# Optimization experiments

Hardware: AMD Instinct MI355X
Metric: run time of the kernel (lower is better)

The kernel has to match this reference:

```python
import jax, jax.numpy as jnp
import numpy as np

BN_EPS = 1e-5


def _knn_idx(pos, k):
    # pos: (B, 3, N). Nearest-k by squared euclidean distance (self included).
    sq = jnp.sum(pos * pos, axis=1)                        # (B, N)
    inner = jnp.einsum('bcn,bcm->bnm', pos, pos)           # (B, N, N)
    neg_dist = 2.0 * inner - sq[:, :, None] - sq[:, None, :]
    _, idx = jax.lax.top_k(neg_dist, k)                    # (B, N, k)
    return idx


def setup_inputs() -> dict:
    key = jax.random.key(0)
    k1, k2, k3 = jax.random.split(key, 3)
    B, C, N, K, D = 4, 64, 8192, 16, 64
    return {
        'x': jax.random.normal(k1, (B, C, N), dtype=jnp.float32),
        'pos': jax.random.normal(k2, (B, 3, N), dtype=jnp.float32),
        'spectral_filter': jax.random.normal(k3, (K, C, D), dtype=jnp.float32),
        'gamma': jnp.ones((D,), dtype=jnp.float32),
        'beta': jnp.zeros((D,), dtype=jnp.float32),
    }


def reference(x, pos, spectral_filter, gamma, beta):
    k = spectral_filter.shape[0]
    idx = _knn_idx(pos, k)                                  # (B, N, k) int32
    # gather neighbors: nb[b, c, n, j] = x[b, c, idx[b, n, j]]
    nb = jax.vmap(lambda xf, ii: xf[:, ii])(x, idx)         # (B, C, N, k)
    edge = nb - x[:, :, :, None]                            # (B, C, N, k)
    # per-k small GEMM: 'bnkc,kcd->bnd' (channel dim is axis 1 here)
    out = jnp.einsum('bcnk,kcd->bnd', edge, spectral_filter)
    out = out.transpose(0, 2, 1)                            # (B, D, N)
    # BatchNorm1d, training mode (biased variance over batch and points)
    mean = jnp.mean(out, axis=(0, 2), keepdims=True)
    var = jnp.var(out, axis=(0, 2), keepdims=True)
    out = (out - mean) * jax.lax.rsqrt(var + BN_EPS)
    return out * gamma[None, :, None] + beta[None, :, None]
```

## Files before the change

kernel.cpp:

```cpp
#include <hip/hip_runtime.h>
#include <hip/hip_bf16.h>

#define NPTS 8192
#define NQ   32768
#define KNN  16
#define SCAP 112

#define OFF_XT   0
#define OFF_FBIG (8*1024*1024)
#define OFF_SUMS (OFF_FBIG + 278528)
#define OFF_IDX  (OFF_SUMS + 512)
#define OFF_PRE  (OFF_IDX + 2*1024*1024)
#define OFF_SQ   OFF_PRE

__device__ __forceinline__ float sq3(float x, float y, float z) {
    #pragma clang fp contract(off)
    float xx = x * x;
    float yy = y * y;
    float zz = z * z;
    return (xx + yy) + zz;
}
__device__ __forceinline__ float negd2(float qx, float qy, float qz, float sqn,
                                       float mx, float my, float mz, float sqm) {
    #pragma clang fp contract(off)
    float p0 = qx * mx;
    float inn = __builtin_fmaf(qz, mz, __builtin_fmaf(qy, my, p0));
    float t = 2.0f * inn;
    float u = t - sqn;
    return u - sqm;
}
#define KEY_EPS2 2.0e-3f

__global__ __launch_bounds__(256) void k_prep(const float* __restrict__ x,
                                              const float* __restrict__ F,
                                              const float* __restrict__ pos,
                                              float* __restrict__ xT,
                                              float* __restrict__ Fb,
                                              float* __restrict__ sums,
                                              float* __restrict__ sqa) {
    int bid = blockIdx.x;
    if (bid < 512) {
        __shared__ float tile[64][65];
        int lane = threadIdx.x & 63, wid = threadIdx.x >> 6;
        int b = bid >> 7, nt = bid & 127;
        int n0 = nt * 64;
        for (int rr = 0; rr < 16; ++rr) {
            int c = wid * 16 + rr;
            tile[c][lane] = x[((size_t)b * 64 + c) * NPTS + n0 + lane];
        }
        __syncthreads();
        for (int rr = 0; rr < 16; ++rr) {
            int r = wid * 16 + rr;
            xT[((size_t)(b * NPTS + n0 + r)) * 64 + lane] = tile[lane][r];
        }
    } else if (bid < 528) {
        int j = bid - 512;
        for (int e = threadIdx.x; e < 4096; e += 256)
            Fb[j * 4096 + e] = F[j * 4096 + e];
    } else if (bid == 528) {
        for (int e = threadIdx.x; e < 4096; e += 256) {
            float s = 0.f;
            for (int k = 0; k < 16; ++k) s += F[k * 4096 + e];
            Fb[16 * 4096 + e] = -s;
        }
    } else if (bid == 529) {
        if (threadIdx.x < 128) sums[threadIdx.x] = 0.f;
    } else {
        int g = (bid - 530) * 256 + threadIdx.x;
        int b = g >> 13, n = g & (NPTS - 1);
        const float* pb = pos + (size_t)b * 3 * NPTS;
        sqa[g] = sq3(pb[n], pb[NPTS + n], pb[2 * NPTS + n]);
    }
}

__global__ __launch_bounds__(256, 8) void k_knn(const float* __restrict__ pos,
                                                const float* __restrict__ sqa,
                                                int* __restrict__ idxo) {
    __shared__ int            cnt[16];
    __shared__ unsigned short sidx[16][SCAP];
    __shared__ float          skey[16][SCAP];
    __shared__ int            outI[16][16];
    int t = threadIdx.x, lane = t & 63, wid = t >> 6;
    int qblk = blockIdx.x * 16;
    int b = qblk >> 13;
    const float* px = pos + (size_t)b * 3 * NPTS;
    const float* py = px + NPTS;
    const float* pz = py + NPTS;
    const float* sb = sqa + (size_t)b * NPTS;
    int n0 = (qblk & (NPTS - 1)) + wid * 4;

    float qxs[4], qys[4], qzs[4], sqs[4], tqx[4], tqy[4], tqz[4];
    #pragma unroll
    for (int i = 0; i < 4; ++i) {
        qxs[i] = px[n0 + i]; qys[i] = py[n0 + i]; qzs[i] = pz[n0 + i];
        sqs[i] = sb[n0 + i];
        tqx[i] = 2.0f * qxs[i]; tqy[i] = 2.0f * qys[i]; tqz[i] = 2.0f * qzs[i];
    }
    if (lane < 4) cnt[wid * 4 + lane] = 0;
    if (lane < 16) {
        #pragma unroll
        for (int i = 0; i < 4; ++i) outI[wid * 4 + i][lane] = n0 + i;
    }

    float lm[4];
    #pragma unroll
    for (int i = 0; i < 4; ++i) lm[i] = -3.4e38f;
    for (int it = 0; it < 32; ++it) {
        int m = it * 256 + lane * 4;
        float4 X = *(const float4*)(px + m);
        float4 Y = *(const float4*)(py + m);
        float4 Z = *(const float4*)(pz + m);
        float4 S = *(const float4*)(sb + m);
        #pragma unroll
        for (int i = 0; i < 4; ++i) {
            float a0 = __builtin_fmaf(tqx[i], X.x, __builtin_fmaf(tqy[i], Y.x, __builtin_fmaf(tqz[i], Z.x, -S.x)));
            float a1 = __builtin_fmaf(tqx[i], X.y, __builtin_fmaf(tqy[i], Y.y, __builtin_fmaf(tqz[i], Z.y, -S.y)));
            float a2 = __builtin_fmaf(tqx[i], X.z, __builtin_fmaf(tqy[i], Y.z, __builtin_fmaf(tqz[i], Z.z, -S.z)));
            float a3 = __builtin_fmaf(tqx[i], X.w, __builtin_fmaf(tqy[i], Y.w, __builtin_fmaf(tqz[i], Z.w, -S.w)));
            float m012 = fmaxf(fmaxf(a0, a1), a2);
            lm[i] = fmaxf(fmaxf(m012, a3), lm[i]);
        }
    }

    float thr[4];
    {
        unsigned up[4], pfx[4];
        #pragma unroll
        for (int i = 0; i < 4; ++i) {
            unsigned s = __float_as_uint(lm[i]);
            up[i]  = s ^ ((unsigned)((int)s >> 31) | 0x80000000u);
            pfx[i] = 0u;
        }
        for (int bit = 31; bit >= 0; --bit) {
            unsigned bmask = 1u << bit;
            #pragma unroll
            for (int i = 0; i < 4; ++i) {
                unsigned trial = pfx[i] | bmask;
                unsigned long long m = __ballot(up[i] >= trial);
                if (__popcll(m) >= 16) pfx[i] = trial;
            }
        }
        #pragma unroll
        for (int i = 0; i < 4; ++i) {
            unsigned p = pfx[i];
            unsigned sbits = (p & 0x80000000u) ? (p ^ 0x80000000u) : ~p;
            thr[i] = __uint_as_float(sbits) - KEY_EPS2;
        }
    }

    for (int it = 0; it < 32; ++it) {
        int m = it * 256 + lane * 4;
        float4 X = *(const float4*)(px + m);
        float4 Y = *(const float4*)(py + m);
        float4 Z = *(const float4*)(pz + m);
        float4 S = *(const float4*)(sb + m);
        #pragma unroll
        for (int i = 0; i < 4; ++i) {
            int lq = wid * 4 + i;
            float a0 = __builtin_fmaf(tqx[i], X.x, __builtin_fmaf(tqy[i], Y.x, __builtin_fmaf(tqz[i], Z.x, -S.x)));
            float a1 = __builtin_fmaf(tqx[i], X.y, __builtin_fmaf(tqy[i], Y.y, __builtin_fmaf(tqz[i], Z.y, -S.y)));
            float a2 = __builtin_fmaf(tqx[i], X.z, __builtin_fmaf(tqy[i], Y.z, __builtin_fmaf(tqz[i], Z.z, -S.z)));
            float a3 = __builtin_fmaf(tqx[i], X.w, __builtin_fmaf(tqy[i], Y.w, __builtin_fmaf(tqz[i], Z.w, -S.w)));
            if (a0 >= thr[i]) { int s_ = atomicAdd(&cnt[lq],1); if (s_<SCAP) sidx[lq][s_] = (unsigned short)m; }
            if (a1 >= thr[i]) { int s_ = atomicAdd(&cnt[lq],1); if (s_<SCAP) sidx[lq][s_] = (unsigned short)(m+1); }
            if (a2 >= thr[i]) { int s_ = atomicAdd(&cnt[lq],1); if (s_<SCAP) sidx[lq][s_] = (unsigned short)(m+2); }
            if (a3 >= thr[i]) { int s_ = atomicAdd(&cnt[lq],1); if (s_<SCAP) sidx[lq][s_] = (unsigned short)(m+3); }
        }
    }

    #pragma unroll 1
    for (int i = 0; i < 4; ++i) {
        int lq = wid * 4 + i;
        int S = cnt[lq]; if (S > SCAP) S = SCAP;
        for (int p = lane; p < S; p += 64) {
            int m = sidx[lq][p];
            skey[lq][p] = negd2(qxs[i], qys[i], qzs[i], sqs[i],
                                px[m], py[m], pz[m], sb[m]);
        }
    }

    #pragma unroll 1
    for (int i = 0; i < 4; ++i) {
        int lq = wid * 4 + i;
        int S = cnt[lq]; if (S > SCAP) S = SCAP;
        for (int p = lane; p < S; p += 64) {
            int m = sidx[lq][p];
            float km = skey[lq][p];
            int rank = 0;
            for (int j = 0; j < S; ++j) {
                float kj = skey[lq][j];
                int ij = sidx[lq][j];
                if (kj > km || (kj == km && ij < m)) rank++;
            }
            if (rank < KNN) outI[lq][rank] = m;
        }
    }
    __syncthreads();
    {
        int lq = t >> 4;
        idxo[(size_t)(qblk + lq) * KNN + (t & 15)] = outI[lq][t & 15];
    }
}

#define CPAD 68
__global__ __launch_bounds__(256) void k_conv(const float* __restrict__ xT,
                                              const float* __restrict__ Fb,
                                              const int* __restrict__ idx,
                                              float* __restrict__ outp,
                                              float* __restrict__ sums) {
    __shared__ float At[64][CPAD];
    __shared__ float Bt[64 * 64];
    int t = threadIdx.x;
    int q0 = blockIdx.x * 64;
    int bbase = q0 & ~(NPTS - 1);
    int qi0 = (t >> 4) * 4;
    int dj0 = (t & 15) * 4;
    int r = t & 63;
    int s = t >> 6;

    float acc[4][4];
    #pragma unroll
    for (int a = 0; a < 4; ++a)
        #pragma unroll
        for (int bb = 0; bb < 4; ++bb) acc[a][bb] = 0.f;

    for (int j = 0; j < 17; ++j) {
        {
            int qg = q0 + r;
            int nbr = (j < 16) ? (idx[(size_t)qg * KNN + j] & (NPTS - 1))
                               : (qg & (NPTS - 1));
            const float* src = xT + ((size_t)(bbase + nbr) * 64 + s * 16);
            float4 v0 = *(const float4*)(src);
            float4 v1 = *(const float4*)(src + 4);
            float4 v2 = *(const float4*)(src + 8);
            float4 v3 = *(const float4*)(src + 12);
            int c0 = s * 16;
            At[c0+ 0][r] = v0.x; At[c0+ 1][r] = v0.y; At[c0+ 2][r] = v0.z; At[c0+ 3][r] = v0.w;
            At[c0+ 4][r] = v1.x; At[c0+ 5][r] = v1.y; At[c0+ 6][r] = v1.z; At[c0+ 7][r] = v1.w;
            At[c0+ 8][r] = v2.x; At[c0+ 9][r] = v2.y; At[c0+10][r] = v2.z; At[c0+11][r] = v2.w;
            At[c0+12][r] = v3.x; At[c0+13][r] = v3.y; At[c0+14][r] = v3.z; At[c0+15][r] = v3.w;
        }
        {
            const float* fj = Fb + j * 4096;
            #pragma unroll
            for (int u = 0; u < 4; ++u) {
                int e = u * 1024 + t * 4;
                *(float4*)&Bt[e] = *(const float4*)(fj + e);
            }
        }
        __syncthreads();
        #pragma unroll 8
        for (int k = 0; k < 64; ++k) {
            float4 av = *(const float4*)&At[k][qi0];
            float4 bv = *(const float4*)&Bt[k * 64 + dj0];
            acc[0][0] = fmaf(av.x, bv.x, acc[0][0]);
            acc[0][1] = fmaf(av.x, bv.y, acc[0][1]);
            acc[0][2] = fmaf(av.x, bv.z, acc[0][2]);
            acc[0][3] = fmaf(av.x, bv.w, acc[0][3]);
            acc[1][0] = fmaf(av.y, bv.x, acc[1][0]);
            acc[1][1] = fmaf(av.y, bv.y, acc[1][1]);
            acc[1][2] = fmaf(av.y, bv.z, acc[1][2]);
            acc[1][3] = fmaf(av.y, bv.w, acc[1][3]);
            acc[2][0] = fmaf(av.z, bv.x, acc[2][0]);
            acc[2][1] = fmaf(av.z, bv.y, acc[2][1]);
            acc[2][2] = fmaf(av.z, bv.z, acc[2][2]);
            acc[2][3] = fmaf(av.z, bv.w, acc[2][3]);
            acc[3][0] = fmaf(av.w, bv.x, acc[3][0]);
            acc[3][1] = fmaf(av.w, bv.y, acc[3][1]);
            acc[3][2] = fmaf(av.w, bv.z, acc[3][2]);
            acc[3][3] = fmaf(av.w, bv.w, acc[3][3]);
        }
        __syncthreads();
    }
    #pragma unroll
    for (int qi = 0; qi < 4; ++qi) {
        float4 o = make_float4(acc[qi][0], acc[qi][1], acc[qi][2], acc[qi][3]);
        *(float4*)(outp + (size_t)(q0 + qi0 + qi) * 64 + dj0) = o;
    }
    {
        float* P  = Bt;
        float* P2 = Bt + 1024;
        int g = t >> 4;
        #pragma unroll
        for (int dd = 0; dd < 4; ++dd) {
            float sv = ((acc[0][dd] + acc[1][dd]) + acc[2][dd]) + acc[3][dd];
            float qv = fmaf(acc[3][dd], acc[3][dd],
                       fmaf(acc[2][dd], acc[2][dd],
                       fmaf(acc[1][dd], acc[1][dd], acc[0][dd] * acc[0][dd])));
            P [g * 64 + dj0 + dd] = sv;
            P2[g * 64 + dj0 + dd] = qv;
        }
        __syncthreads();
        if (t < 64) {
            float a = 0.f, b2 = 0.f;
            #pragma unroll
            for (int gg = 0; gg < 16; ++gg) {
                a  += P [gg * 64 + t];
                b2 += P2[gg * 64 + t];
            }
            atomicAdd(&sums[t], a);
            atomicAdd(&sums[64 + t], b2);
        }
    }
}

__global__ __launch_bounds__(256) void k_bn(const float* __restrict__ outp,
                                            const float* __restrict__ sums,
                                            const float* __restrict__ gamma,
                                            const float* __restrict__ beta,
                                            float* __restrict__ out) {
    __shared__ float tile[64][65];
    __shared__ float sa[64], sb[64];
    int lane = threadIdx.x & 63, wid = threadIdx.x >> 6;
    int b = blockIdx.x >> 7, nt = blockIdx.x & 127;
    int n0 = nt * 64;
    if (threadIdx.x < 64) {
        const float inv = 1.f / 32768.f;
        float mean = sums[threadIdx.x] * inv;
        float var = sums[64 + threadIdx.x] * inv - mean * mean;
        float rs = rsqrtf(var + 1e-5f);
        float a = rs * gamma[threadIdx.x];
        sa[threadIdx.x] = a;
        sb[threadIdx.x] = beta[threadIdx.x] - mean * a;
    }
    for (int rr = 0; rr < 16; ++rr) {
        int r = wid * 16 + rr;
        tile[r][lane] = outp[((size_t)(b * NPTS + n0 + r)) * 64 + lane];
    }
    __syncthreads();
    for (int rr = 0; rr < 16; ++rr) {
        int dr = wid * 16 + rr;
        out[((size_t)b * 64 + dr) * NPTS + n0 + lane] =
            fmaf(tile[lane][dr], sa[dr], sb[dr]);
    }
}

extern "C" void kernel_launch(void* const* d_in, const int* in_sizes, int n_in,
                              void* d_out, int out_size, void* d_ws, size_t ws_size,
                              hipStream_t stream) {
    (void)in_sizes; (void)n_in; (void)out_size; (void)ws_size;
    const float* x     = (const float*)d_in[0];
    const float* pos   = (const float*)d_in[1];
    const float* F     = (const float*)d_in[2];
    const float* gamma = (const float*)d_in[3];
    const float* beta  = (const float*)d_in[4];
    float* out = (float*)d_out;

    char* ws = (char*)d_ws;
    float* xT   = (float*)(ws + OFF_XT);
    float* Fb   = (float*)(ws + OFF_FBIG);
    float* sums = (float*)(ws + OFF_SUMS);
    int*   idx  = (int*)(ws + OFF_IDX);
    float* pre  = (float*)(ws + OFF_PRE);
    float* sqa  = (float*)(ws + OFF_SQ);

    k_prep<<<658, 256, 0, stream>>>(x, F, pos, xT, Fb, sums, sqa);
    k_knn<<<2048, 256, 0, stream>>>(pos, sqa, idx);
    k_conv<<<512, 256, 0, stream>>>(xT, Fb, idx, pre, sums);
    k_bn<<<512, 256, 0, stream>>>(pre, sums, gamma, beta, out);
}
```

Baseline: 259.2 us.

## Fuse kNN threshold and collection passes with progressive threshold refinement

The kNN kernel used to make two full passes over all 8192 points: one to find per-lane maxima for a top-16 threshold, and one to collect candidates above it. Now only the first 1024 points set an initial threshold. A single pass over the rest then both collects candidates and keeps updating the lane maxima, recomputing the threshold at two later checkpoints. This roughly halves the global loads and FMA work of the scan. In exchange, early loose thresholds admit more candidates, so the candidate buffer grows from 112 to 160 entries, raising LDS use and risking overflow that would drop true neighbours.

```diff
diff --git a/kernel.cpp b/kernel.cpp
--- a/kernel.cpp
+++ b/kernel.cpp
@@ -4,7 +4,7 @@
 #define NPTS 8192
 #define NQ   32768
 #define KNN  16
-#define SCAP 112
+#define SCAP 160
 
 #define OFF_XT   0
 #define OFF_FBIG (8*1024*1024)
@@ -73,6 +73,31 @@
     }
 }
 
+__device__ __forceinline__ void sel16(const float* lm, float* thr) {
+    unsigned up[4], pfx[4];
+    #pragma unroll
+    for (int i = 0; i < 4; ++i) {
+        unsigned s = __float_as_uint(lm[i]);
+        up[i]  = s ^ ((unsigned)((int)s >> 31) | 0x80000000u);
+        pfx[i] = 0u;
+    }
+    for (int bit = 31; bit >= 0; --bit) {
+        unsigned bmask = 1u << bit;
+        #pragma unroll
+        for (int i = 0; i < 4; ++i) {
+            unsigned trial = pfx[i] | bmask;
+            unsigned long long m = __ballot(up[i] >= trial);
+            if (__popcll(m) >= 16) pfx[i] = trial;
+        }
+    }
+    #pragma unroll
+    for (int i = 0; i < 4; ++i) {
+        unsigned p = pfx[i];
+        unsigned sbits = (p & 0x80000000u) ? (p ^ 0x80000000u) : ~p;
+        thr[i] = __uint_as_float(sbits) - KEY_EPS2;
+    }
+}
+
 __global__ __launch_bounds__(256, 8) void k_knn(const float* __restrict__ pos,
                                                 const float* __restrict__ sqa,
                                                 int* __restrict__ idxo) {
@@ -89,12 +114,11 @@
     const float* sb = sqa + (size_t)b * NPTS;
     int n0 = (qblk & (NPTS - 1)) + wid * 4;
 
-    float qxs[4], qys[4], qzs[4], sqs[4], tqx[4], tqy[4], tqz[4];
-    #pragma unroll
-    for (int i = 0; i < 4; ++i) {
-        qxs[i] = px[n0 + i]; qys[i] = py[n0 + i]; qzs[i] = pz[n0 + i];
+    float sqs[4], tqx[4], tqy[4], tqz[4];
+    #pragma unroll
+    for (int i = 0; i < 4; ++i) {
         sqs[i] = sb[n0 + i];
-        tqx[i] = 2.0f * qxs[i]; tqy[i] = 2.0f * qys[i]; tqz[i] = 2.0f * qzs[i];
+        tqx[i] = 2.0f * px[n0 + i]; tqy[i] = 2.0f * py[n0 + i]; tqz[i] = 2.0f * pz[n0 + i];
     }
     if (lane < 4) cnt[wid * 4 + lane] = 0;
     if (lane < 16) {
@@ -105,7 +129,8 @@
     float lm[4];
     #pragma unroll
     for (int i = 0; i < 4; ++i) lm[i] = -3.4e38f;
-    for (int it = 0; it < 32; ++it) {
+
+    for (int it = 0; it < 4; ++it) {
         int m = it * 256 + lane * 4;
         float4 X = *(const float4*)(px + m);
         float4 Y = *(const float4*)(py + m);
@@ -123,32 +148,9 @@
     }
 
     float thr[4];
-    {
-        unsigned up[4], pfx[4];
-        #pragma unroll
-        for (int i = 0; i < 4; ++i) {
-            unsigned s = __float_as_uint(lm[i]);
-            up[i]  = s ^ ((unsigned)((int)s >> 31) | 0x80000000u);
-            pfx[i] = 0u;
-        }
-        for (int bit = 31; bit >= 0; --bit) {
-            unsigned bmask = 1u << bit;
-            #pragma unroll
-            for (int i = 0; i < 4; ++i) {
-                unsigned trial = pfx[i] | bmask;
-                unsigned long long m = __ballot(up[i] >= trial);
-                if (__popcll(m) >= 16) pfx[i] = trial;
-            }
-        }
-        #pragma unroll
-        for (int i = 0; i < 4; ++i) {
-            unsigned p = pfx[i];
-            unsigned sbits = (p & 0x80000000u) ? (p ^ 0x80000000u) : ~p;
-            thr[i] = __uint_as_float(sbits) - KEY_EPS2;
-        }
-    }
-
-    for (int it = 0; it < 32; ++it) {
+    sel16(lm, thr);
+
+    for (int it = 0; it < 4; ++it) {
         int m = it * 256 + lane * 4;
         float4 X = *(const float4*)(px + m);
         float4 Y = *(const float4*)(py + m);
@@ -168,13 +170,37 @@
         }
     }
 
+    for (int it = 4; it < 32; ++it) {
+        if (it == 8 || it == 16) sel16(lm, thr);
+        int m = it * 256 + lane * 4;
+        float4 X = *(const float4*)(px + m);
+        float4 Y = *(const float4*)(py + m);
+        float4 Z = *(const float4*)(pz + m);
+        float4 S = *(const float4*)(sb + m);
+        #pragma unroll
+        for (int i = 0; i < 4; ++i) {
+            int lq = wid * 4 + i;
+            float a0 = __builtin_fmaf(tqx[i], X.x, __builtin_fmaf(tqy[i], Y.x, __builtin_fmaf(tqz[i], Z.x, -S.x)));
+            float a1 = __builtin_fmaf(tqx[i], X.y, __builtin_fmaf(tqy[i], Y.y, __builtin_fmaf(tqz[i], Z.y, -S.y)));
+            float a2 = __builtin_fmaf(tqx[i], X.z, __builtin_fmaf(tqy[i], Y.z, __builtin_fmaf(tqz[i], Z.z, -S.z)));
+            float a3 = __builtin_fmaf(tqx[i], X.w, __builtin_fmaf(tqy[i], Y.w, __builtin_fmaf(tqz[i], Z.w, -S.w)));
+            float m012 = fmaxf(fmaxf(a0, a1), a2);
+            lm[i] = fmaxf(fmaxf(m012, a3), lm[i]);
+            if (a0 >= thr[i]) { int s_ = atomicAdd(&cnt[lq],1); if (s_<SCAP) sidx[lq][s_] = (unsigned short)m; }
+            if (a1 >= thr[i]) { int s_ = atomicAdd(&cnt[lq],1); if (s_<SCAP) sidx[lq][s_] = (unsigned short)(m+1); }
+            if (a2 >= thr[i]) { int s_ = atomicAdd(&cnt[lq],1); if (s_<SCAP) sidx[lq][s_] = (unsigned short)(m+2); }
+            if (a3 >= thr[i]) { int s_ = atomicAdd(&cnt[lq],1); if (s_<SCAP) sidx[lq][s_] = (unsigned short)(m+3); }
+        }
+    }
+
     #pragma unroll 1
     for (int i = 0; i < 4; ++i) {
         int lq = wid * 4 + i;
         int S = cnt[lq]; if (S > SCAP) S = SCAP;
+        float qx = 0.5f * tqx[i], qy = 0.5f * tqy[i], qz = 0.5f * tqz[i];
         for (int p = lane; p < S; p += 64) {
             int m = sidx[lq][p];
-            skey[lq][p] = negd2(qxs[i], qys[i], qzs[i], sqs[i],
+            skey[lq][p] = negd2(qx, qy, qz, sqs[i],
                                 px[m], py[m], pz[m], sb[m]);
         }
     }
```

Result: slower. 370.2 us (+42.8%).

## Split kNN point scan across waves, each wave handling all 16 queries

Applied to the files above, without the earlier changes.

Each of the four waves in a block now scans a quarter of the candidate points for all 16 queries, instead of scanning every point for its own 4 queries. Per-lane maxima go into a shared buffer that is unioned with the candidate lists, then are combined per query before the ballot-based threshold search. Candidate collection uses shared atomics across waves, with extra block barriers between phases. This cuts redundant loads of the point arrays per block but raises register pressure (16 query coordinate sets, 16 maxima, 16 thresholds) and adds synchronisation.

```diff
diff --git a/kernel.cpp b/kernel.cpp
--- a/kernel.cpp
+++ b/kernel.cpp
@@ -30,6 +30,10 @@
     return u - sqm;
 }
 #define KEY_EPS2 2.0e-3f
+
+__device__ __forceinline__ float rfl(float v) {
+    return __uint_as_float(__builtin_amdgcn_readfirstlane(__float_as_uint(v)));
+}
 
 __global__ __launch_bounds__(256) void k_prep(const float* __restrict__ x,
                                               const float* __restrict__ F,
@@ -73,13 +77,44 @@
     }
 }
 
+__device__ __forceinline__ void sel16(const float* lm, float* thr) {
+    unsigned up[4], pfx[4];
+    #pragma unroll
+    for (int i = 0; i < 4; ++i) {
+        unsigned s = __float_as_uint(lm[i]);
+        up[i]  = s ^ ((unsigned)((int)s >> 31) | 0x80000000u);
+        pfx[i] = 0u;
+    }
+    for (int bit = 31; bit >= 0; --bit) {
+        unsigned bmask = 1u << bit;
+        #pragma unroll
+        for (int i = 0; i < 4; ++i) {
+            unsigned trial = pfx[i] | bmask;
+            unsigned long long m = __ballot(up[i] >= trial);
+            if (__popcll(m) >= 16) pfx[i] = trial;
+        }
+    }
+    #pragma unroll
+    for (int i = 0; i < 4; ++i) {
+        unsigned p = pfx[i];
+        unsigned sbits = (p & 0x80000000u) ? (p ^ 0x80000000u) : ~p;
+        thr[i] = __uint_as_float(sbits) - KEY_EPS2;
+    }
+}
+
 __global__ __launch_bounds__(256, 8) void k_knn(const float* __restrict__ pos,
                                                 const float* __restrict__ sqa,
                                                 int* __restrict__ idxo) {
-    __shared__ int            cnt[16];
-    __shared__ unsigned short sidx[16][SCAP];
-    __shared__ float          skey[16][SCAP];
-    __shared__ int            outI[16][16];
+    __shared__ int   cnt[16];
+    __shared__ int   outI[16][16];
+    __shared__ float thrs[16];
+    __shared__ union {
+        float lm[16][256];
+        struct {
+            unsigned short sidx[16][SCAP];
+            float          skey[16][SCAP];
+        } ab;
+    } sh;
     int t = threadIdx.x, lane = t & 63, wid = t >> 6;
     int qblk = blockIdx.x * 16;
     int b = qblk >> 13;
@@ -87,32 +122,33 @@
     const float* py = px + NPTS;
     const float* pz = py + NPTS;
     const float* sb = sqa + (size_t)b * NPTS;
-    int n0 = (qblk & (NPTS - 1)) + wid * 4;
-
-    float qxs[4], qys[4], qzs[4], sqs[4], tqx[4], tqy[4], tqz[4];
-    #pragma unroll
-    for (int i = 0; i < 4; ++i) {
-        qxs[i] = px[n0 + i]; qys[i] = py[n0 + i]; qzs[i] = pz[n0 + i];
-        sqs[i] = sb[n0 + i];
-        tqx[i] = 2.0f * qxs[i]; tqy[i] = 2.0f * qys[i]; tqz[i] = 2.0f * qzs[i];
+    int qn = qblk & (NPTS - 1);
+
+    float tqx[16], tqy[16], tqz[16];
+    #pragma unroll
+    for (int i = 0; i < 16; ++i) {
+        tqx[i] = rfl(2.0f * px[qn + i]);
+        tqy[i] = rfl(2.0f * py[qn + i]);
+        tqz[i] = rfl(2.0f * pz[qn + i]);
     }
     if (lane < 4) cnt[wid * 4 + lane] = 0;
     if (lane < 16) {
         #pragma unroll
-        for (int i = 0; i < 4; ++i) outI[wid * 4 + i][lane] = n0 + i;
-    }
-
-    float lm[4];
-    #pragma unroll
-    for (int i = 0; i < 4; ++i) lm[i] = -3.4e38f;
-    for (int it = 0; it < 32; ++it) {
-        int m = it * 256 + lane * 4;
+        for (int i = 0; i < 4; ++i) outI[wid * 4 + i][lane] = qn + wid * 4 + i;
+    }
+
+    float lm[16];
+    #pragma unroll
+    for (int i = 0; i < 16; ++i) lm[i] = -3.4e38f;
+    int base = wid * 2048;
+    for (int it = 0; it < 8; ++it) {
+        int m = base + it * 256 + lane * 4;
         float4 X = *(const float4*)(px + m);
         float4 Y = *(const float4*)(py + m);
         float4 Z = *(const float4*)(pz + m);
         float4 S = *(const float4*)(sb + m);
         #pragma unroll
-        for (int i = 0; i < 4; ++i) {
+        for (int i = 0; i < 16; ++i) {
             float a0 = __builtin_fmaf(tqx[i], X.x, __builtin_fmaf(tqy[i], Y.x, __builtin_fmaf(tqz[i], Z.x, -S.x)));
             float a1 = __builtin_fmaf(tqx[i], X.y, __builtin_fmaf(tqy[i], Y.y, __builtin_fmaf(tqz[i], Z.y, -S.y)));
             float a2 = __builtin_fmaf(tqx[i], X.z, __builtin_fmaf(tqy[i], Y.z, __builtin_fmaf(tqz[i], Z.z, -S.z)));
@@ -121,75 +157,81 @@
             lm[i] = fmaxf(fmaxf(m012, a3), lm[i]);
         }
     }
-
-    float thr[4];
+    #pragma unroll
+    for (int i = 0; i < 16; ++i) sh.lm[i][wid * 64 + lane] = lm[i];
+    __syncthreads();
+
     {
-        unsigned up[4], pfx[4];
-        #pragma unroll
-        for (int i = 0; i < 4; ++i) {
-            unsigned s = __float_as_uint(lm[i]);
-            up[i]  = s ^ ((unsigned)((int)s >> 31) | 0x80000000u);
-            pfx[i] = 0u;
-        }
-        for (int bit = 31; bit >= 0; --bit) {
-            unsigned bmask = 1u << bit;
+        float comb[4];
+        #pragma unroll
+        for (int j = 0; j < 4; ++j) {
+            int i = wid * 4 + j;
+            float c0 = sh.lm[i][lane];
+            float c1 = sh.lm[i][64 + lane];
+            float c2 = sh.lm[i][128 + lane];
+            float c3 = sh.lm[i][192 + lane];
+            comb[j] = fmaxf(fmaxf(c0, c1), fmaxf(c2, c3));
+        }
+        float thr4[4];
+        sel16(comb, thr4);
+        if (lane < 4) thrs[wid * 4 + lane] = thr4[lane];
+        if (lane == 0) {
             #pragma unroll
-            for (int i = 0; i < 4; ++i) {
-                unsigned trial = pfx[i] | bmask;
-                unsigned long long m = __ballot(up[i] >= trial);
-                if (__popcll(m) >= 16) pfx[i] = trial;
-            }
-        }
-        #pragma unroll
-        for (int i = 0; i < 4; ++i) {
-            unsigned p = pfx[i];
-            unsigned sbits = (p & 0x80000000u) ? (p ^ 0x80000000u) : ~p;
-            thr[i] = __uint_as_float(sbits) - KEY_EPS2;
-        }
-    }
-
-    for (int it = 0; it < 32; ++it) {
-        int m = it * 256 + lane * 4;
+            for (int j = 0; j < 4; ++j) thrs[wid * 4 + j] = thr4[j];
+        }
+    }
+    __syncthreads();
+    float thr[16];
+    #pragma unroll
+    for (int i = 0; i < 16; ++i) thr[i] = thrs[i];
+
+    for (int it = 0; it < 8; ++it) {
+        int m = base + it * 256 + lane * 4;
         float4 X = *(const float4*)(px + m);
         float4 Y = *(const float4*)(py + m);
         float4 Z = *(const float4*)(pz + m);
         float4 S = *(const float4*)(sb + m);
         #pragma unroll
-        for (int i = 0; i < 4; ++i) {
-            int lq = wid * 4 + i;
+        for (int i = 0; i < 16; ++i) {
             float a0 = __builtin_fmaf(tqx[i], X.x, __builtin_fmaf(tqy[i], Y.x, __builtin_fmaf(tqz[i], Z.x, -S.x)));
             float a1 = __builtin_fmaf(tqx[i], X.y, __builtin_fmaf(tqy[i], Y.y, __builtin_fmaf(tqz[i], Z.y, -S.y)));
             float a2 = __builtin_fmaf(tqx[i], X.z, __builtin_fmaf(tqy[i], Y.z, __builtin_fmaf(tqz[i], Z.z, -S.z)));
             float a3 = __builtin_fmaf(tqx[i], X.w, __builtin_fmaf(tqy[i], Y.w, __builtin_fmaf(tqz[i], Z.w, -S.w)));
-            if (a0 >= thr[i]) { int s_ = atomicAdd(&cnt[lq],1); if (s_<SCAP) sidx[lq][s_] = (unsigned short)m; }
-            if (a1 >= thr[i]) { int s_ = atomicAdd(&cnt[lq],1); if (s_<SCAP) sidx[lq][s_] = (unsigned short)(m+1); }
-            if (a2 >= thr[i]) { int s_ = atomicAdd(&cnt[lq],1); if (s_<SCAP) sidx[lq][s_] = (unsigned short)(m+2); }
-            if (a3 >= thr[i]) { int s_ = atomicAdd(&cnt[lq],1); if (s_<SCAP) sidx[lq][s_] = (unsigned short)(m+3); }
-        }
-    }
+            if (a0 >= thr[i]) { int s_ = atomicAdd(&cnt[i],1); if (s_<SCAP) sh.ab.sidx[i][s_] = (unsigned short)m; }
+            if (a1 >= thr[i]) { int s_ = atomicAdd(&cnt[i],1); if (s_<SCAP) sh.ab.sidx[i][s_] = (unsigned short)(m+1); }
+            if (a2 >= thr[i]) { int s_ = atomicAdd(&cnt[i],1); if (s_<SCAP) sh.ab.sidx[i][s_] = (unsigned short)(m+2); }
+            if (a3 >= thr[i]) { int s_ = atomicAdd(&cnt[i],1); if (s_<SCAP) sh.ab.sidx[i][s_] = (unsigned short)(m+3); }
+        }
+    }
+    __syncthreads();
+
+    #pragma unroll 1
+    for (int i = 0; i < 4; ++i) {
+        int lq = wid * 4 + i;
+        int S = cnt[lq]; if (S > SCAP) S = SCAP;
+        float qx = 0.5f * tqx[0];
+        (void)qx;
+        float qxx = 0.5f * tqx[lq], qyy = 0.5f * tqy[lq], qzz = 0.5f * tqz[lq];
+        float sqn = sb[qn + lq];
+        for (int p = lane; p < S; p += 64) {
+            int m = sh.ab.sidx[lq][p];
+            sh.ab.skey[lq][p] = negd2(qxx, qyy, qzz, sqn,
+                                      px[m], py[m], pz[m], sb[m]);
+        }
+    }
+    __syncthreads();
 
     #pragma unroll 1
     for (int i = 0; i < 4; ++i) {
         int lq = wid * 4 + i;
         int S = cnt[lq]; if (S > SCAP) S = SCAP;
         for (int p = lane; p < S; p += 64) {
-            int m = sidx[lq][p];
-            skey[lq][p] = negd2(qxs[i], qys[i], qzs[i], sqs[i],
-                                px[m], py[m], pz[m], sb[m]);
-        }
-    }
-
-    #pragma unroll 1
-    for (int i = 0; i < 4; ++i) {
-        int lq = wid * 4 + i;
-        int S = cnt[lq]; if (S > SCAP) S = SCAP;
-        for (int p = lane; p < S; p += 64) {
-            int m = sidx[lq][p];
-            float km = skey[lq][p];
+            int m = sh.ab.sidx[lq][p];
+            float km = sh.ab.skey[lq][p];
             int rank = 0;
             for (int j = 0; j < S; ++j) {
-                float kj = skey[lq][j];
-                int ij = sidx[lq][j];
+                float kj = sh.ab.skey[lq][j];
+                int ij = sh.ab.sidx[lq][j];
                 if (kj > km || (kj == km && ij < m)) rank++;
             }
             if (rank < KNN) outI[lq][rank] = m;
```

New measurement: 804.6 us. 3.1x slower.
